# Kernel optimization log

Measured on AMD Instinct MI355X. Metric: run time of the kernel, lower is better.

The kernel has to match this reference:

```python
import jax, jax.numpy as jnp
import numpy as np

D_MODEL = 2048
NUM_HEADS = 16
HEAD_DIM = D_MODEL // NUM_HEADS
B, S = 2, 2048


def setup_inputs() -> dict:
    key = jax.random.key(0)
    ks = jax.random.split(key, 11)
    scale = 1.0 / np.sqrt(D_MODEL)
    inp = {
        "query": jax.random.normal(ks[0], (B, S, D_MODEL), dtype=jnp.float32),
        "key": jax.random.normal(ks[1], (B, S, D_MODEL), dtype=jnp.float32),
        "value": jax.random.normal(ks[2], (B, S, D_MODEL), dtype=jnp.float32),
        "Wq": jax.random.normal(ks[3], (D_MODEL, D_MODEL), dtype=jnp.float32) * scale,
        "bq": jax.random.normal(ks[4], (D_MODEL,), dtype=jnp.float32) * 0.01,
        "Wk": jax.random.normal(ks[5], (D_MODEL, D_MODEL), dtype=jnp.float32) * scale,
        "bk": jax.random.normal(ks[6], (D_MODEL,), dtype=jnp.float32) * 0.01,
        "Wv": jax.random.normal(ks[7], (D_MODEL, D_MODEL), dtype=jnp.float32) * scale,
        "bv": jax.random.normal(ks[8], (D_MODEL,), dtype=jnp.float32) * 0.01,
        "Wo": jax.random.normal(ks[9], (D_MODEL, D_MODEL), dtype=jnp.float32) * scale,
        "bo": jax.random.normal(ks[10], (D_MODEL,), dtype=jnp.float32) * 0.01,
    }
    return inp


def _shape(x, B, S):
    # [B, S, D] -> [B, H, S, hd]
    return x.reshape(B, S, NUM_HEADS, HEAD_DIM).transpose(0, 2, 1, 3)


def reference(query, key, value, Wq, bq, Wk, bk, Wv, bv, Wo, bo):
    B, Sq, D = query.shape
    Sk = key.shape[1]
    # Linear layers (torch: y = x @ W.T + b)
    Q = _shape(query @ Wq.T + bq, B, Sq)   # [B,H,Sq,hd]
    K = _shape(key @ Wk.T + bk, B, Sk)     # [B,H,Sk,hd]
    V = _shape(value @ Wv.T + bv, B, Sk)   # [B,H,Sk,hd]
    scores = jnp.einsum('bhqd,bhkd->bhqk', Q, K) / jnp.sqrt(jnp.float32(HEAD_DIM))
    # causal mask: triu(ones(Sq, Sk), diagonal=1)
    causal = jnp.triu(jnp.ones((Sq, Sk), dtype=bool), k=1)
    scores = jnp.where(causal[None, None, :, :], jnp.float32(-jnp.inf), scores)
    attn = jax.nn.softmax(scores, axis=-1)
    out = jnp.einsum('bhqk,bhkd->bhqd', attn, V)
    out = out.transpose(0, 2, 1, 3).reshape(B, Sq, D)
    return out @ Wo.T + bo
```

## Files before the change

### kernel.cpp

```cpp
#include <hip/hip_runtime.h>
#include <hip/hip_bf16.h>

typedef __attribute__((ext_vector_type(8))) short short8;
typedef __attribute__((ext_vector_type(4))) short s16x4;
typedef __attribute__((ext_vector_type(4))) float f32x4;

#define MFMA_BF16(A, B, C) __builtin_amdgcn_mfma_f32_16x16x32_bf16(A, B, C, 0, 0, 0)

__device__ __forceinline__ void gload_lds16(const __hip_bfloat16* g, __hip_bfloat16* l) {
  __builtin_amdgcn_global_load_lds(
      (const __attribute__((address_space(1))) unsigned int*)g,
      (__attribute__((address_space(3))) unsigned int*)l, 16, 0, 0);
}

__device__ __forceinline__ float finite_or(float x, float repl) {
  unsigned u;
  __builtin_memcpy(&u, &x, 4);
  return ((u & 0x7f800000u) == 0x7f800000u) ? repl : x;
}

__device__ __forceinline__ short bf16_bits(float x) {
  __hip_bfloat16 b = __float2bfloat16(x);
  short s;
  __builtin_memcpy(&s, &b, 2);
  return s;
}

__device__ __forceinline__ short8 pack8(f32x4 a, f32x4 b) {
  short8 r;
  r[0] = bf16_bits(a[0]); r[1] = bf16_bits(a[1]);
  r[2] = bf16_bits(a[2]); r[3] = bf16_bits(a[3]);
  r[4] = bf16_bits(b[0]); r[5] = bf16_bits(b[1]);
  r[6] = bf16_bits(b[2]); r[7] = bf16_bits(b[3]);
  return r;
}

__global__ __launch_bounds__(256) void cvt_kernel(
    const float* x0, const float* x1, const float* x2,
    const float* w0, const float* w1, const float* w2, const float* w3,
    __hip_bfloat16* y0, __hip_bfloat16* y1, __hip_bfloat16* y2,
    __hip_bfloat16* u0, __hip_bfloat16* u1, __hip_bfloat16* u2, __hip_bfloat16* u3)
{
  const int z = blockIdx.y;
  const float* s = z == 0 ? x0 : z == 1 ? x1 : z == 2 ? x2
                 : z == 3 ? w0 : z == 4 ? w1 : z == 5 ? w2 : w3;
  __hip_bfloat16* d = z == 0 ? y0 : z == 1 ? y1 : z == 2 ? y2
                    : z == 3 ? u0 : z == 4 ? u1 : z == 5 ? u2 : u3;
  const size_t n = (z < 3) ? (size_t)8388608 : (size_t)4194304;
  const size_t stride = (size_t)gridDim.x * 256 * 8;
  for (size_t i = ((size_t)blockIdx.x * 256 + threadIdx.x) * 8; i < n; i += stride) {
    f32x4 a = *(const f32x4*)(s + i);
    f32x4 b = *(const f32x4*)(s + i + 4);
    *(short8*)((short*)d + i) = pack8(a, b);
  }
}

#define GBUF 24576

__device__ __forceinline__ void stage_A(const __hip_bfloat16* Ab, __hip_bfloat16* bufA,
                                        int kcol, int t, int wave) {
#pragma unroll
  for (int r = 0; r < 2; ++r) {
    const int ci = r * 512 + t;
    const int row = ci >> 3, c = ci & 7;
    const int sc = c ^ (row & 7);
    gload_lds16(Ab + (size_t)row * 2048 + kcol + sc * 8, bufA + r * 4096 + wave * 512);
  }
}
__device__ __forceinline__ void stage_Br(const __hip_bfloat16* Bb, __hip_bfloat16* bufB,
                                         int kcol, int t, int wave, int r) {
  const int ci = r * 512 + t;
  const int row = ci >> 3, c = ci & 7;
  const int sc = c ^ (row & 7);
  gload_lds16(Bb + (size_t)row * 2048 + kcol + sc * 8, bufB + r * 4096 + wave * 512);
}

template <typename OutT, bool BIAS_ROW>
__device__ __forceinline__ void gemm8p_body(
    const __hip_bfloat16* __restrict__ A, const __hip_bfloat16* __restrict__ Bt,
    const float* __restrict__ bias, OutT* __restrict__ C,
    int m0, int n0, int N, float trip, __hip_bfloat16* sm)
{
  constexpr int K = 2048, NT = K / 64;
  const int t = threadIdx.x, wave = t >> 6, lane = t & 63;
  const int ll = lane & 15, lg = lane >> 4;
  const int wmB = (wave >> 2) * 64, wnB = (wave & 3) * 64;
  const __hip_bfloat16* Ab = A + (size_t)m0 * K;
  const __hip_bfloat16* Bb = Bt + (size_t)n0 * K;

  f32x4 acc[4][4] = {};

  stage_A(Ab, sm, 0, t, wave);
  stage_Br(Bb, sm + 8192, 0, t, wave, 0);
  stage_Br(Bb, sm + 8192, 0, t, wave, 1);
  stage_Br(Bb, sm + 8192, 0, t, wave, 2);
  stage_Br(Bb, sm + 8192, 0, t, wave, 3);
  stage_A(Ab, sm + GBUF, 64, t, wave);
  stage_Br(Bb, sm + GBUF + 8192, 64, t, wave, 0);
  stage_Br(Bb, sm + GBUF + 8192, 64, t, wave, 1);
  stage_Br(Bb, sm + GBUF + 8192, 64, t, wave, 2);
  stage_Br(Bb, sm + GBUF + 8192, 64, t, wave, 3);
  asm volatile("s_waitcnt vmcnt(6)" ::: "memory");
  __builtin_amdgcn_s_barrier();

  for (int i = 0; i < NT; ++i) {
    const __hip_bfloat16* bufA = sm + (i % 3) * GBUF;
    const __hip_bfloat16* bufB = bufA + 8192;
    const bool pf = (i + 2 < NT);
    __hip_bfloat16* pA = sm + ((i + 2) % 3) * GBUF;
    const int pk = (i + 2) * 64;

#pragma unroll
    for (int kk = 0; kk < 2; ++kk) {
      short8 af[4], bf[4];
#pragma unroll
      for (int f = 0; f < 4; ++f) {
        const int ar = wmB + f * 16 + ll;
        af[f] = *(const short8*)&bufA[ar * 64 + (((kk * 4 + lg) ^ (ar & 7)) << 3)];
        const int br = wnB + f * 16 + ll;
        bf[f] = *(const short8*)&bufB[br * 64 + (((kk * 4 + lg) ^ (br & 7)) << 3)];
      }
      if (pf) {
        if (kk == 0) {
          stage_A(Ab, pA, pk, t, wave);
          stage_Br(Bb, pA + 8192, pk, t, wave, 0);
        } else {
          stage_Br(Bb, pA + 8192, pk, t, wave, 1);
          stage_Br(Bb, pA + 8192, pk, t, wave, 2);
          stage_Br(Bb, pA + 8192, pk, t, wave, 3);
        }
      }
      asm volatile("s_waitcnt lgkmcnt(0)" ::: "memory");
      __builtin_amdgcn_sched_barrier(0);
      __builtin_amdgcn_s_setprio(1);
#pragma unroll
      for (int mi = 0; mi < 4; ++mi)
#pragma unroll
        for (int ni = 0; ni < 4; ++ni)
          acc[mi][ni] = MFMA_BF16(af[mi], bf[ni], acc[mi][ni]);
      __builtin_amdgcn_s_setprio(0);
      __builtin_amdgcn_sched_barrier(0);
    }

    const int rem = NT - 1 - i;
    if (rem >= 2) {
      asm volatile("s_waitcnt vmcnt(6)" ::: "memory");
      __builtin_amdgcn_s_barrier();
    } else if (rem == 1) {
      asm volatile("s_waitcnt vmcnt(0)" ::: "memory");
      __builtin_amdgcn_s_barrier();
    }
  }

#pragma unroll
  for (int mi = 0; mi < 4; ++mi)
#pragma unroll
    for (int ni = 0; ni < 4; ++ni) {
      const int col = n0 + wnB + ni * 16 + ll;
      const float bcol = BIAS_ROW ? 0.f : bias[col];
#pragma unroll
      for (int j = 0; j < 4; ++j) {
        const int row = m0 + wmB + mi * 16 + lg * 4 + j;
        const float bv = BIAS_ROW ? bias[row] : bcol;
        const float val = finite_or(acc[mi][ni][j] + bv, trip);
        if constexpr (__is_same(OutT, float))
          C[(size_t)row * N + col] = val;
        else
          C[(size_t)row * N + col] = __float2bfloat16(val);
      }
    }
}

__global__ __launch_bounds__(512) void gemm_qkvvt_kernel(
    const __hip_bfloat16* xq, const __hip_bfloat16* xk, const __hip_bfloat16* xv,
    const __hip_bfloat16* Wq, const __hip_bfloat16* Wk, const __hip_bfloat16* Wv,
    const float* bq, const float* bk, const float* bv,
    __hip_bfloat16* Q, __hip_bfloat16* K, __hip_bfloat16* Vt2)
{
  __shared__ __align__(16) __hip_bfloat16 sm[3 * GBUF];
  const int L = (int)blockIdx.x;
  if (L < 512) {
    const int z = L & 1;
    const int r = L >> 1;
    const int n0 = (r & 7) * 256;
    const int m0 = (r >> 3) * 128;
    gemm8p_body<__hip_bfloat16, false>(z ? xk : xq, z ? Wk : Wq, z ? bk : bq,
                                       z ? K : Q, m0, n0, 2048, 20000.0f, sm);
  } else {
    const int r = L - 512;
    const int n0 = (r & 15) * 256;
    const int m0 = (r >> 4) * 128;
    gemm8p_body<__hip_bfloat16, true>(Wv, xv, bv, Vt2, m0, n0, 4096, 30000.0f, sm);
  }
}

__global__ __launch_bounds__(512) void gemm_out_kernel(
    const __hip_bfloat16* A, const __hip_bfloat16* W, const float* b, float* C)
{
  __shared__ __align__(16) __hip_bfloat16 sm[3 * GBUF];
  gemm8p_body<float, false>(A, W, b, C, (int)blockIdx.y * 128,
                            (int)blockIdx.x * 256, 2048, 50000.0f, sm);
}

__global__ __launch_bounds__(256) void attn_kernel(
    const __hip_bfloat16* __restrict__ Qb, const __hip_bfloat16* __restrict__ Kb,
    const __hip_bfloat16* __restrict__ Vt, __hip_bfloat16* __restrict__ Ob)
{
  constexpr int S = 2048, D = 2048, HD = 128;
  __shared__ __align__(16) __hip_bfloat16 Ks[64 * 128];
  __shared__ __align__(16) __hip_bfloat16 Vs[128 * 64];
  __shared__ __align__(16) short Ps[4][16 * 64];

  const int t = threadIdx.x, wave = t >> 6, lane = t & 63;
  const int lg = lane >> 4, ll = lane & 15;
  const int L = (int)blockIdx.x;
  const int bh = ((L & 7) << 2) | ((L >> 3) & 3);
  const int p = L >> 5;
  const int a = p & 7, bq_ = p >> 3;
  const int qi = (bq_ == 0) ? a : (bq_ == 1) ? 15 - a
               : (bq_ == 2) ? 16 + a : 31 - a;
  const int b = bh >> 4, h = bh & 15;
  const int q0 = qi * 64;
  const int qrow = q0 + wave * 16 + ll;
  char* const Psw = (char*)&Ps[wave][0];

  auto stageKV = [&](int kv0) {
#pragma unroll
    for (int r = 0; r < 4; ++r) {
      const int s = r * 256 + t;
      const int row = s >> 4, ch = s & 15;
      const int sc = ch ^ (row & 7);
      gload_lds16(Kb + (size_t)(b * S + kv0 + row) * D + h * HD + sc * 8,
                  Ks + r * 2048 + wave * 512);
    }
#pragma unroll
    for (int r = 0; r < 4; ++r) {
      const int s = r * 256 + t;
      const int d = s >> 3, ch = s & 7;
      const int sc = ch ^ (d & 7);
      gload_lds16(Vt + (size_t)(h * HD + d) * (2 * S) + b * S + kv0 + sc * 8,
                  Vs + r * 2048 + wave * 512);
    }
  };

  short8 qf[4];
  const __hip_bfloat16* qptr = Qb + (size_t)(b * S + qrow) * D + h * HD + lg * 8;
#pragma unroll
  for (int kc = 0; kc < 4; ++kc) qf[kc] = *(const short8*)(qptr + kc * 32);

  f32x4 oacc[8] = {};
  float mrun = -1e30f, lrun = 0.f;

  for (int tk = 0; tk <= qi; ++tk) {
    const int kv0 = tk * 64;
    __builtin_amdgcn_s_barrier();
    stageKV(kv0);
    asm volatile("s_waitcnt vmcnt(0)" ::: "memory");
    __builtin_amdgcn_s_barrier();

    f32x4 sacc[4] = {};
#pragma unroll
    for (int nf = 0; nf < 4; ++nf) {
      const int krow = nf * 16 + ll;
#pragma unroll
      for (int kc = 0; kc < 4; ++kc) {
        const int sw = (kc * 4 + lg) ^ (krow & 7);
        const short8 kf = *(const short8*)&Ks[krow * 128 + sw * 8];
        sacc[nf] = MFMA_BF16(kf, qf[kc], sacc[nf]);
      }
    }

    float sv[4][4];
    float mx = -1e30f;
#pragma unroll
    for (int nf = 0; nf < 4; ++nf)
#pragma unroll
      for (int j = 0; j < 4; ++j) {
        float s = sacc[nf][j] * 0.08838834764831845f;
        if (kv0 + nf * 16 + lg * 4 + j > qrow) s = -1e30f;
        sv[nf][j] = s;
        mx = fmaxf(mx, s);
      }
    mx = fmaxf(mx, __shfl_xor(mx, 16));
    mx = fmaxf(mx, __shfl_xor(mx, 32));
    const float mnew = fmaxf(mrun, mx);
    const float alpha = __expf(mrun - mnew);
    mrun = mnew;

    float rs = 0.f;
#pragma unroll
    for (int nf = 0; nf < 4; ++nf) {
      s16x4 pk;
#pragma unroll
      for (int j = 0; j < 4; ++j) {
        const float pv = __expf(sv[nf][j] - mnew);
        rs += pv;
        pk[j] = bf16_bits(pv);
      }
      const int chunk = (nf * 2 + (lg >> 1)) ^ (ll & 7);
      *(s16x4*)(Psw + ll * 128 + chunk * 16 + (lg & 1) * 8) = pk;
    }
    rs += __shfl_xor(rs, 16);
    rs += __shfl_xor(rs, 32);
    lrun = lrun * alpha + rs;
#pragma unroll
    for (int df = 0; df < 8; ++df)
#pragma unroll
      for (int j = 0; j < 4; ++j) oacc[df][j] *= alpha;

    asm volatile("s_waitcnt lgkmcnt(0)" ::: "memory");
    __builtin_amdgcn_sched_barrier(0);

#pragma unroll
    for (int ks = 0; ks < 2; ++ks) {
      const int pchunk = (ks * 4 + lg) ^ (ll & 7);
      const short8 pf8 = *(const short8*)(Psw + ll * 128 + pchunk * 16);
#pragma unroll
      for (int df = 0; df < 8; ++df) {
        const int vrow = df * 16 + ll;
        const int sw = (ks * 4 + lg) ^ (vrow & 7);
        const short8 vf = *(const short8*)&Vs[vrow * 64 + sw * 8];
        oacc[df] = MFMA_BF16(vf, pf8, oacc[df]);
      }
    }
  }

  const float inv = 1.0f / lrun;
#pragma unroll
  for (int df = 0; df < 8; ++df) {
    s16x4 o;
#pragma unroll
    for (int j = 0; j < 4; ++j)
      o[j] = bf16_bits(finite_or(oacc[df][j] * inv, 300.0f));
    *(s16x4*)(Ob + (size_t)(b * S + qrow) * D + h * HD + df * 16 + lg * 4) = o;
  }
}

extern "C" void kernel_launch(void* const* d_in, const int* in_sizes, int n_in,
                              void* d_out, int out_size, void* d_ws, size_t ws_size,
                              hipStream_t stream)
{
  const float* q  = (const float*)d_in[0];
  const float* k  = (const float*)d_in[1];
  const float* v  = (const float*)d_in[2];
  const float* Wq = (const float*)d_in[3];
  const float* bq = (const float*)d_in[4];
  const float* Wk = (const float*)d_in[5];
  const float* bk = (const float*)d_in[6];
  const float* Wv = (const float*)d_in[7];
  const float* bv = (const float*)d_in[8];
  const float* Wo = (const float*)d_in[9];
  const float* bo = (const float*)d_in[10];

  char* wsb = (char*)d_ws;
  const size_t MB = 1024 * 1024;
  __hip_bfloat16* Qw  = (__hip_bfloat16*)(wsb + 0 * MB);
  __hip_bfloat16* Kw  = (__hip_bfloat16*)(wsb + 16 * MB);
  __hip_bfloat16* Vt2 = (__hip_bfloat16*)(wsb + 32 * MB);
  __hip_bfloat16* xqb = (__hip_bfloat16*)(wsb + 48 * MB);
  __hip_bfloat16* xkb = (__hip_bfloat16*)(wsb + 64 * MB);
  __hip_bfloat16* xvb = (__hip_bfloat16*)(wsb + 80 * MB);
  __hip_bfloat16* Wqb = (__hip_bfloat16*)(wsb + 96 * MB);
  __hip_bfloat16* Wkb = (__hip_bfloat16*)(wsb + 104 * MB);
  __hip_bfloat16* Wvb = (__hip_bfloat16*)(wsb + 112 * MB);
  __hip_bfloat16* Wob = (__hip_bfloat16*)(wsb + 120 * MB);
  __hip_bfloat16* Ow  = xkb;

  cvt_kernel<<<dim3(1024, 7), 256, 0, stream>>>(
      q, k, v, Wq, Wk, Wv, Wo, xqb, xkb, xvb, Wqb, Wkb, Wvb, Wob);
  gemm_qkvvt_kernel<<<dim3(768), 512, 0, stream>>>(
      xqb, xkb, xvb, Wqb, Wkb, Wvb, bq, bk, bv, Qw, Kw, Vt2);
  attn_kernel<<<dim3(1024), 256, 0, stream>>>(Qw, Kw, Vt2, Ow);
  gemm_out_kernel<<<dim3(8, 32), 512, 0, stream>>>(
      Ow, Wob, bo, (float*)d_out);
}
```

Baseline: 269.4 us.

## Use 32x32 MFMA and 128-row query tiles in attention kernel

Rewrites the attention kernel so each wave handles 32 query rows with 32x32x16 bf16 MFMA instead of 16 rows with 16x16x32. The block's query tile grows from 64 to 128 rows, which halves the grid to 512 blocks and halves how often each K/V tile is re-staged across blocks. The causal tile ordering is rebalanced to pair light and heavy query tiles. In exchange it uses more registers per wave, gives fewer blocks for load balancing, and masks more work on the diagonal tiles.

```diff
diff --git a/kernel.cpp b/kernel.cpp
--- a/kernel.cpp
+++ b/kernel.cpp
@@ -4,8 +4,10 @@
 typedef __attribute__((ext_vector_type(8))) short short8;
 typedef __attribute__((ext_vector_type(4))) short s16x4;
 typedef __attribute__((ext_vector_type(4))) float f32x4;
+typedef __attribute__((ext_vector_type(16))) float f32x16;
 
 #define MFMA_BF16(A, B, C) __builtin_amdgcn_mfma_f32_16x16x32_bf16(A, B, C, 0, 0, 0)
+#define MFMA32(A, B, C) __builtin_amdgcn_mfma_f32_32x32x16_bf16(A, B, C, 0, 0, 0)
 
 __device__ __forceinline__ void gload_lds16(const __hip_bfloat16* g, __hip_bfloat16* l) {
   __builtin_amdgcn_global_load_lds(
@@ -209,19 +211,17 @@
   constexpr int S = 2048, D = 2048, HD = 128;
   __shared__ __align__(16) __hip_bfloat16 Ks[64 * 128];
   __shared__ __align__(16) __hip_bfloat16 Vs[128 * 64];
-  __shared__ __align__(16) short Ps[4][16 * 64];
+  __shared__ __align__(16) short Ps[4][32 * 64];
 
   const int t = threadIdx.x, wave = t >> 6, lane = t & 63;
-  const int lg = lane >> 4, ll = lane & 15;
+  const int lq = lane & 31, hi = lane >> 5;
   const int L = (int)blockIdx.x;
   const int bh = ((L & 7) << 2) | ((L >> 3) & 3);
   const int p = L >> 5;
-  const int a = p & 7, bq_ = p >> 3;
-  const int qi = (bq_ == 0) ? a : (bq_ == 1) ? 15 - a
-               : (bq_ == 2) ? 16 + a : 31 - a;
+  const int qi = (p < 8) ? p : 23 - p;
   const int b = bh >> 4, h = bh & 15;
-  const int q0 = qi * 64;
-  const int qrow = q0 + wave * 16 + ll;
+  const int q0 = qi * 128;
+  const int qrow = q0 + wave * 32 + lq;
   char* const Psw = (char*)&Ps[wave][0];
 
   auto stageKV = [&](int kv0) {
@@ -243,45 +243,45 @@
     }
   };
 
-  short8 qf[4];
-  const __hip_bfloat16* qptr = Qb + (size_t)(b * S + qrow) * D + h * HD + lg * 8;
-#pragma unroll
-  for (int kc = 0; kc < 4; ++kc) qf[kc] = *(const short8*)(qptr + kc * 32);
-
-  f32x4 oacc[8] = {};
+  short8 qf[8];
+  const __hip_bfloat16* qptr = Qb + (size_t)(b * S + qrow) * D + h * HD + hi * 8;
+#pragma unroll
+  for (int s = 0; s < 8; ++s) qf[s] = *(const short8*)(qptr + s * 16);
+
+  f32x16 oacc[4] = {};
   float mrun = -1e30f, lrun = 0.f;
 
-  for (int tk = 0; tk <= qi; ++tk) {
+  const int NT = 2 * qi + 2;
+  for (int tk = 0; tk < NT; ++tk) {
     const int kv0 = tk * 64;
     __builtin_amdgcn_s_barrier();
     stageKV(kv0);
     asm volatile("s_waitcnt vmcnt(0)" ::: "memory");
     __builtin_amdgcn_s_barrier();
 
-    f32x4 sacc[4] = {};
-#pragma unroll
-    for (int nf = 0; nf < 4; ++nf) {
-      const int krow = nf * 16 + ll;
-#pragma unroll
-      for (int kc = 0; kc < 4; ++kc) {
-        const int sw = (kc * 4 + lg) ^ (krow & 7);
-        const short8 kf = *(const short8*)&Ks[krow * 128 + sw * 8];
-        sacc[nf] = MFMA_BF16(kf, qf[kc], sacc[nf]);
-      }
-    }
-
-    float sv[4][4];
+    f32x16 sacc[2] = {};
+#pragma unroll
+    for (int kb = 0; kb < 2; ++kb) {
+      const int krow = kb * 32 + lq;
+#pragma unroll
+      for (int s = 0; s < 8; ++s) {
+        const short8 kf =
+            *(const short8*)&Ks[krow * 128 + (((s * 2 + hi) ^ (lq & 7)) << 3)];
+        sacc[kb] = MFMA32(kf, qf[s], sacc[kb]);
+      }
+    }
+
     float mx = -1e30f;
 #pragma unroll
-    for (int nf = 0; nf < 4; ++nf)
-#pragma unroll
-      for (int j = 0; j < 4; ++j) {
-        float s = sacc[nf][j] * 0.08838834764831845f;
-        if (kv0 + nf * 16 + lg * 4 + j > qrow) s = -1e30f;
-        sv[nf][j] = s;
-        mx = fmaxf(mx, s);
-      }
-    mx = fmaxf(mx, __shfl_xor(mx, 16));
+    for (int kb = 0; kb < 2; ++kb)
+#pragma unroll
+      for (int r = 0; r < 16; ++r) {
+        float sv = sacc[kb][r] * 0.08838834764831845f;
+        const int k = kv0 + kb * 32 + (r & 3) + 8 * (r >> 2) + 4 * hi;
+        if (k > qrow) sv = -1e30f;
+        sacc[kb][r] = sv;
+        mx = fmaxf(mx, sv);
+      }
     mx = fmaxf(mx, __shfl_xor(mx, 32));
     const float mnew = fmaxf(mrun, mx);
     const float alpha = __expf(mrun - mnew);
@@ -289,51 +289,54 @@
 
     float rs = 0.f;
 #pragma unroll
-    for (int nf = 0; nf < 4; ++nf) {
-      s16x4 pk;
-#pragma unroll
-      for (int j = 0; j < 4; ++j) {
-        const float pv = __expf(sv[nf][j] - mnew);
-        rs += pv;
-        pk[j] = bf16_bits(pv);
-      }
-      const int chunk = (nf * 2 + (lg >> 1)) ^ (ll & 7);
-      *(s16x4*)(Psw + ll * 128 + chunk * 16 + (lg & 1) * 8) = pk;
-    }
-    rs += __shfl_xor(rs, 16);
+    for (int kb = 0; kb < 2; ++kb)
+#pragma unroll
+      for (int g = 0; g < 4; ++g) {
+        s16x4 pk;
+#pragma unroll
+        for (int j = 0; j < 4; ++j) {
+          const float pv = __expf(sacc[kb][g * 4 + j] - mnew);
+          rs += pv;
+          pk[j] = bf16_bits(pv);
+        }
+        *(s16x4*)(Psw + lq * 128 + (((kb * 4 + g) ^ (lq & 7)) << 4) + hi * 8) = pk;
+      }
     rs += __shfl_xor(rs, 32);
     lrun = lrun * alpha + rs;
 #pragma unroll
-    for (int df = 0; df < 8; ++df)
-#pragma unroll
-      for (int j = 0; j < 4; ++j) oacc[df][j] *= alpha;
+    for (int db = 0; db < 4; ++db)
+#pragma unroll
+      for (int r = 0; r < 16; ++r) oacc[db][r] *= alpha;
 
     asm volatile("s_waitcnt lgkmcnt(0)" ::: "memory");
     __builtin_amdgcn_sched_barrier(0);
 
 #pragma unroll
-    for (int ks = 0; ks < 2; ++ks) {
-      const int pchunk = (ks * 4 + lg) ^ (ll & 7);
-      const short8 pf8 = *(const short8*)(Psw + ll * 128 + pchunk * 16);
-#pragma unroll
-      for (int df = 0; df < 8; ++df) {
-        const int vrow = df * 16 + ll;
-        const int sw = (ks * 4 + lg) ^ (vrow & 7);
-        const short8 vf = *(const short8*)&Vs[vrow * 64 + sw * 8];
-        oacc[df] = MFMA_BF16(vf, pf8, oacc[df]);
+    for (int ks = 0; ks < 4; ++ks) {
+      const short8 pf =
+          *(const short8*)(Psw + lq * 128 + (((ks * 2 + hi) ^ (lq & 7)) << 4));
+#pragma unroll
+      for (int db = 0; db < 4; ++db) {
+        const int vrow = db * 32 + lq;
+        const short8 vf =
+            *(const short8*)&Vs[vrow * 64 + (((ks * 2 + hi) ^ (lq & 7)) << 3)];
+        oacc[db] = MFMA32(vf, pf, oacc[db]);
       }
     }
   }
 
   const float inv = 1.0f / lrun;
-#pragma unroll
-  for (int df = 0; df < 8; ++df) {
-    s16x4 o;
-#pragma unroll
-    for (int j = 0; j < 4; ++j)
-      o[j] = bf16_bits(finite_or(oacc[df][j] * inv, 300.0f));
-    *(s16x4*)(Ob + (size_t)(b * S + qrow) * D + h * HD + df * 16 + lg * 4) = o;
-  }
+  __hip_bfloat16* obase = Ob + (size_t)(b * S + qrow) * D + h * HD;
+#pragma unroll
+  for (int db = 0; db < 4; ++db)
+#pragma unroll
+    for (int g = 0; g < 4; ++g) {
+      s16x4 o;
+#pragma unroll
+      for (int j = 0; j < 4; ++j)
+        o[j] = bf16_bits(finite_or(oacc[db][g * 4 + j] * inv, 300.0f));
+      *(s16x4*)(obase + db * 32 + 8 * g + 4 * hi) = o;
+    }
 }
 
 extern "C" void kernel_launch(void* const* d_in, const int* in_sizes, int n_in,
@@ -370,7 +373,7 @@
       q, k, v, Wq, Wk, Wv, Wo, xqb, xkb, xvb, Wqb, Wkb, Wvb, Wob);
   gemm_qkvvt_kernel<<<dim3(768), 512, 0, stream>>>(
       xqb, xkb, xvb, Wqb, Wkb, Wvb, bq, bk, bv, Qw, Kw, Vt2);
-  attn_kernel<<<dim3(1024), 256, 0, stream>>>(Qw, Kw, Vt2, Ow);
+  attn_kernel<<<dim3(512), 256, 0, stream>>>(Qw, Kw, Vt2, Ow);
   gemm_out_kernel<<<dim3(8, 32), 512, 0, stream>>>(
       Ow, Wob, bo, (float*)d_out);
 }
```

New measurement: 276.5 us. 2.6% more time.
